# Optimization experiments

Measured on AMD Instinct MI355X. Metric: run time of the kernel, lower is better.

Reference implementation:

```python
import jax, jax.numpy as jnp
import numpy as np
import math

N_HEADS = 16
SINK_STRENGTH = 0.1


def setup_inputs() -> dict:
    key = jax.random.key(0)
    ks = jax.random.split(key, 16)
    B, S, D = 2, 2048, 1024
    sd = 1.0 / math.sqrt(D)
    return {
        "query": jax.random.normal(ks[0], (B, S, D), jnp.float32),
        "key_": jax.random.normal(ks[1], (B, S, D), jnp.float32),
        "value": jax.random.normal(ks[2], (B, S, D), jnp.float32),
        "positions": jax.random.uniform(ks[3], (B, S), jnp.float32),
        "attention_mask": jnp.ones((B, S), jnp.int32),
        "Wq": jax.random.normal(ks[4], (D, D), jnp.float32) * sd,
        "bq": jnp.zeros((D,), jnp.float32),
        "Wk": jax.random.normal(ks[5], (D, D), jnp.float32) * sd,
        "bk": jnp.zeros((D,), jnp.float32),
        "Wv": jax.random.normal(ks[6], (D, D), jnp.float32) * sd,
        "bv": jnp.zeros((D,), jnp.float32),
        "Wo": jax.random.normal(ks[7], (D, D), jnp.float32) * sd,
        "bo": jnp.zeros((D,), jnp.float32),
    }


def reference(query, key_, value, positions, attention_mask, Wq, bq, Wk, bk, Wv, bv, Wo, bo):
    B, S, D = query.shape
    H = N_HEADS
    hd = D // H
    scale = 1.0 / math.sqrt(hd)

    def split_heads(x):  # [B,S,D] -> [B,H,S,hd]
        return x.reshape(B, S, H, hd).transpose(0, 2, 1, 3)

    q = split_heads(query @ Wq.T + bq)
    k = split_heads(key_ @ Wk.T + bk)
    v = split_heads(value @ Wv.T + bv)

    scores = jnp.einsum("bhqd,bhkd->bhqk", q, k) * scale  # [B,H,S,S]

    # sink index: argmin of positions over valid (mask!=0) tokens, per batch
    masked_pos = jnp.where(attention_mask == 0, jnp.inf, positions)
    sink_indices = jnp.argmin(masked_pos, axis=-1)  # [B]

    # per-batch sink bias: add sink_strength to every score column at sink index
    sink_onehot = jax.nn.one_hot(sink_indices, S, dtype=scores.dtype)  # [B,S]
    scores = scores + SINK_STRENGTH * sink_onehot[:, None, None, :]

    # key-side padding mask
    scores = jnp.where(attention_mask[:, None, None, :] == 0, -1e9, scores)

    probs = jax.nn.softmax(scores, axis=-1)
    out = jnp.einsum("bhqk,bhkd->bhqd", probs, v)  # [B,H,S,hd]
    out = out.transpose(0, 2, 1, 3).reshape(B, S, D)
    return out @ Wo.T + bo, sink_indices
```

## Files before the change

### kernel.cpp

```cpp
#include <hip/hip_runtime.h>
#include <hip/hip_bf16.h>
#include <math.h>

constexpr int B  = 2;
constexpr int S  = 2048;
constexpr int D  = 1024;
constexpr int H  = 16;
constexpr int HD = 64;
constexpr float SCALE = 0.125f;
constexpr float SINK_STRENGTH = 0.1f;

typedef short v4s __attribute__((ext_vector_type(4)));
typedef short v8s __attribute__((ext_vector_type(8)));
typedef float v4f __attribute__((ext_vector_type(4)));

__device__ inline v4f mfma_16x16x32_bf16(v8s a, v8s b, v4f c) {
  return __builtin_amdgcn_mfma_f32_16x16x32_bf16(a, b, c, 0, 0, 0);
}

__device__ inline v4f mfma_16x16x16_bf16(v4s a, v4s b, v4f c) {
#if defined(__has_builtin)
#if __has_builtin(__builtin_amdgcn_mfma_f32_16x16x16bf16_1k)
  return __builtin_amdgcn_mfma_f32_16x16x16bf16_1k(a, b, c, 0, 0, 0);
#define MFMA16_DONE 1
#endif
#endif
#ifndef MFMA16_DONE
  v4f d;
  asm volatile("v_mfma_f32_16x16x16_bf16 %0, %1, %2, %3"
               : "=v"(d) : "v"(a), "v"(b), "v"(c));
  return d;
#endif
}

__device__ inline unsigned short f2bf(float f) {
  __hip_bfloat16 h = __float2bfloat16(f);
  return *reinterpret_cast<unsigned short*>(&h);
}

__device__ inline ushort4 pack4(float4 f) {
  return make_ushort4(f2bf(f.x), f2bf(f.y), f2bf(f.z), f2bf(f.w));
}

__device__ inline void gld16(const void* g, void* l) {
  __builtin_amdgcn_global_load_lds(
      (const __attribute__((address_space(1))) void*)g,
      (__attribute__((address_space(3))) void*)l, 16, 0, 0);
}

__device__ inline void stage8(const unsigned char* gbase, size_t gstride,
                              unsigned char* ldsbase, int rb, int lane) {
  const int r = rb + (lane >> 3);
  const int c = (lane & 7) * 16;
  const unsigned char* g = gbase + (size_t)r * gstride + (c ^ ((r & 7) << 4));
  gld16(g, ldsbase + rb * 128);
}

__device__ inline unsigned swz(int row, int bytecol) {
  return (unsigned)(row * 128 + (bytecol ^ ((row & 7) << 4)));
}

struct CvtArgs {
  const float* src[7];
  unsigned short* dst[7];
  int n[7];
};

__global__ __launch_bounds__(256) void convert_kernel(CvtArgs a) {
  const int t = blockIdx.y;
  const float* s = a.src[t];
  unsigned short* d = a.dst[t];
  const int n = a.n[t];
  for (int i = (blockIdx.x * 256 + threadIdx.x) * 8; i < n;
       i += gridDim.x * 256 * 8) {
    float4 f0 = *reinterpret_cast<const float4*>(s + i);
    float4 f1 = *reinterpret_cast<const float4*>(s + i + 4);
    *reinterpret_cast<ushort4*>(d + i)     = pack4(f0);
    *reinterpret_cast<ushort4*>(d + i + 4) = pack4(f1);
  }
}

__global__ void sink_kernel(const float* __restrict__ pos,
                            const int* __restrict__ mask,
                            int* __restrict__ sink_idx,
                            float* __restrict__ sbias_g,
                            float* __restrict__ out_tail, int tail_elems) {
  const int b = blockIdx.x;
  __shared__ float sval[256];
  __shared__ int   sidx[256];
  float best = INFINITY;
  int   bidx = 0x7fffffff;
  for (int i = threadIdx.x; i < S; i += 256) {
    float v = (mask[b * S + i] == 0) ? INFINITY : pos[b * S + i];
    if (v < best || (v == best && i < bidx)) { best = v; bidx = i; }
  }
  sval[threadIdx.x] = best;
  sidx[threadIdx.x] = bidx;
  __syncthreads();
  for (int off = 128; off > 0; off >>= 1) {
    if ((int)threadIdx.x < off) {
      float v  = sval[threadIdx.x + off];
      int   ix = sidx[threadIdx.x + off];
      if (v < sval[threadIdx.x] ||
          (v == sval[threadIdx.x] && ix < sidx[threadIdx.x])) {
        sval[threadIdx.x] = v;
        sidx[threadIdx.x] = ix;
      }
    }
    __syncthreads();
  }
  const int sb = sidx[0];
  if (threadIdx.x == 0) {
    sink_idx[b] = sb;
    if (b < tail_elems) out_tail[b] = (float)sb;
  }
  for (int i = threadIdx.x; i < S; i += 256)
    sbias_g[b * S + i] =
        mask[b * S + i] ? ((i == sb) ? SINK_STRENGTH : 0.f) : -1e9f;
}

template <int MODE>
__global__ __launch_bounds__(256) void gemm_bf16(
    const unsigned short* __restrict__ X,
    const unsigned short* __restrict__ Wb,
    const float* __restrict__ bias,
    void* __restrict__ Yv, int M, int N, int K) {
  __shared__ __align__(16) unsigned char lds[2 * 24576];
  const int tid = threadIdx.x, lane = tid & 63, w = tid >> 6;
  const int wr = w >> 1, wc = w & 1, lr = lane & 15, g = lane >> 4;
  const int m0 = blockIdx.y * 128, n0 = blockIdx.x * 64;
  const unsigned char* xg = (const unsigned char*)(X + (size_t)m0 * K);
  const unsigned char* wg = (const unsigned char*)(Wb + (size_t)n0 * K);
  const size_t stride = (size_t)K * 2;

  auto stage = [&](int buf, int k0) {
    unsigned char* Xs = lds + buf * 24576;
    unsigned char* Ws = Xs + 16384;
    const unsigned char* xk = xg + k0 * 2;
    const unsigned char* wk = wg + k0 * 2;
#pragma unroll
    for (int u = 0; u < 4; ++u) stage8(xk, stride, Xs, w * 32 + u * 8, lane);
#pragma unroll
    for (int u = 0; u < 2; ++u) stage8(wk, stride, Ws, w * 16 + u * 8, lane);
  };

  stage(0, 0);
  v4f acc[4][2] = {};
  const int ksteps = K / 64;
  int cur = 0;
  for (int s = 0; s < ksteps; ++s) {
    __syncthreads();
    if (s + 1 < ksteps) stage(cur ^ 1, (s + 1) * 64);
    const unsigned char* Xs = lds + cur * 24576;
    const unsigned char* Ws = Xs + 16384;
    const int sw = (lr & 7) << 4;
#pragma unroll
    for (int ks = 0; ks < 2; ++ks) {
      v8s a[4], bf2[2];
#pragma unroll
      for (int mf = 0; mf < 4; ++mf)
        a[mf] = *reinterpret_cast<const v8s*>(
            Xs + (wr * 64 + mf * 16 + lr) * 128 + ((ks * 64 + g * 16) ^ sw));
#pragma unroll
      for (int nf = 0; nf < 2; ++nf)
        bf2[nf] = *reinterpret_cast<const v8s*>(
            Ws + (wc * 32 + nf * 16 + lr) * 128 + ((ks * 64 + g * 16) ^ sw));
#pragma unroll
      for (int mf = 0; mf < 4; ++mf)
#pragma unroll
        for (int nf = 0; nf < 2; ++nf)
          acc[mf][nf] = mfma_16x16x32_bf16(a[mf], bf2[nf], acc[mf][nf]);
    }
    cur ^= 1;
  }

  if constexpr (MODE == 2) {
    float* Y = (float*)Yv;
#pragma unroll
    for (int nf = 0; nf < 2; ++nf) {
      const int n = n0 + wc * 32 + nf * 16 + lr;
      const float bs = bias[n];
#pragma unroll
      for (int mf = 0; mf < 4; ++mf)
#pragma unroll
        for (int r = 0; r < 4; ++r)
          Y[(size_t)(m0 + wr * 64 + mf * 16 + g * 4 + r) * N + n] =
              acc[mf][nf][r] + bs;
    }
  } else if constexpr (MODE == 0) {
    unsigned short* Y = (unsigned short*)Yv;
#pragma unroll
    for (int nf = 0; nf < 2; ++nf) {
      const int n = n0 + wc * 32 + nf * 16 + lr;
      const float bs = bias[n];
#pragma unroll
      for (int mf = 0; mf < 4; ++mf)
#pragma unroll
        for (int r = 0; r < 4; ++r)
          Y[(size_t)(m0 + wr * 64 + mf * 16 + g * 4 + r) * N + n] =
              f2bf(acc[mf][nf][r] + bs);
    }
  } else {
    unsigned short* Y = (unsigned short*)Yv;
#pragma unroll
    for (int nf = 0; nf < 2; ++nf) {
      const int n = n0 + wc * 32 + nf * 16 + lr;
      const int hh = n >> 6, dd = n & 63;
      const float bs = bias[n];
#pragma unroll
      for (int mf = 0; mf < 4; ++mf) {
        const int m = m0 + wr * 64 + mf * 16 + g * 4;
        const int bb = m >> 11, ss = m & 2047;
        float4 f = make_float4(acc[mf][nf][0] + bs, acc[mf][nf][1] + bs,
                               acc[mf][nf][2] + bs, acc[mf][nf][3] + bs);
        *reinterpret_cast<ushort4*>(
            &Y[(((size_t)bb * H + hh) * HD + dd) * S + ss]) = pack4(f);
      }
    }
  }
}

__global__ __launch_bounds__(256) void attn_kernel(
    const unsigned short* __restrict__ qg, const unsigned short* __restrict__ kg,
    const unsigned short* __restrict__ vt, const float* __restrict__ sbias_g,
    unsigned short* __restrict__ og) {
  __shared__ __align__(16) unsigned char smem[8192 + 2 * 16384];
  const int b = blockIdx.z, h = blockIdx.y, q0 = blockIdx.x * 64;
  const int tid = threadIdx.x, lane = tid & 63, wv = tid >> 6;
  const int lr = lane & 15, g = lane >> 4;

  const unsigned char* qgb =
      (const unsigned char*)(qg + ((size_t)b * S + q0) * D + h * HD);
  const unsigned char* kgb0 =
      (const unsigned char*)(kg + (size_t)b * S * D + h * HD);
  const unsigned char* vtb =
      (const unsigned char*)(vt + ((size_t)b * H + h) * HD * S);

  stage8(qgb, D * 2, smem, wv * 16, lane);
  stage8(qgb, D * 2, smem, wv * 16 + 8, lane);
  {
    unsigned char* Ks = smem + 8192;
    unsigned char* Vs = Ks + 8192;
    stage8(kgb0, D * 2, Ks, wv * 16, lane);
    stage8(kgb0, D * 2, Ks, wv * 16 + 8, lane);
    stage8(vtb, S * 2, Vs, wv * 16, lane);
    stage8(vtb, S * 2, Vs, wv * 16 + 8, lane);
  }

  float m_i = -INFINITY, l_i = 0.f;
  v4f acc[4] = {};
  v8s qf[2];
  int cur = 0;

  for (int kv0 = 0; kv0 < S; kv0 += 64) {
    __syncthreads();
    const unsigned char* Ks = smem + 8192 + cur * 16384;
    const unsigned char* Vs = Ks + 8192;

    float4 b4[4];
#pragma unroll
    for (int t = 0; t < 4; ++t)
      b4[t] = *reinterpret_cast<const float4*>(
          &sbias_g[b * S + kv0 + t * 16 + g * 4]);

    if (kv0 + 64 < S) {
      unsigned char* Kn = smem + 8192 + (cur ^ 1) * 16384;
      unsigned char* Vn = Kn + 8192;
      const unsigned char* kgb = kgb0 + (size_t)(kv0 + 64) * (D * 2);
      const unsigned char* vgb = vtb + (size_t)(kv0 + 64) * 2;
      stage8(kgb, D * 2, Kn, wv * 16, lane);
      stage8(kgb, D * 2, Kn, wv * 16 + 8, lane);
      stage8(vgb, S * 2, Vn, wv * 16, lane);
      stage8(vgb, S * 2, Vn, wv * 16 + 8, lane);
    }

    if (kv0 == 0) {
      qf[0] = *reinterpret_cast<const v8s*>(smem + swz(wv * 16 + lr, g * 16));
      qf[1] = *reinterpret_cast<const v8s*>(
          smem + swz(wv * 16 + lr, 64 + g * 16));
    }

    v4f st[4] = {};
#pragma unroll
    for (int t = 0; t < 4; ++t) {
#pragma unroll
      for (int ks = 0; ks < 2; ++ks) {
        v8s aK = *reinterpret_cast<const v8s*>(
            Ks + swz(t * 16 + lr, ks * 64 + g * 16));
        st[t] = mfma_16x16x32_bf16(aK, qf[ks], st[t]);
      }
    }

    float s[4][4];
    float mx = -INFINITY;
#pragma unroll
    for (int t = 0; t < 4; ++t) {
      const float bb[4] = {b4[t].x, b4[t].y, b4[t].z, b4[t].w};
#pragma unroll
      for (int r = 0; r < 4; ++r) {
        s[t][r] = fmaf(st[t][r], SCALE, bb[r]);
        mx = fmaxf(mx, s[t][r]);
      }
    }
    mx = fmaxf(mx, __shfl_xor(mx, 16, 64));
    mx = fmaxf(mx, __shfl_xor(mx, 32, 64));

    const float mn   = fmaxf(m_i, mx);
    const float corr = __expf(m_i - mn);
    float rs = 0.f;
    v4s pb[4];
#pragma unroll
    for (int t = 0; t < 4; ++t) {
#pragma unroll
      for (int r = 0; r < 4; ++r) {
        float pv = __expf(s[t][r] - mn);
        rs += pv;
        pb[t][r] = (short)f2bf(pv);
      }
    }
    rs += __shfl_xor(rs, 16, 64);
    rs += __shfl_xor(rs, 32, 64);
    l_i = l_i * corr + rs;
    m_i = mn;
#pragma unroll
    for (int c = 0; c < 4; ++c) acc[c] = acc[c] * corr;

#pragma unroll
    for (int t = 0; t < 4; ++t) {
#pragma unroll
      for (int c = 0; c < 4; ++c) {
        v4s aV = *reinterpret_cast<const v4s*>(
            Vs + swz(c * 16 + lr, t * 32 + g * 8));
        acc[c] = mfma_16x16x16_bf16(aV, pb[t], acc[c]);
      }
    }
    cur ^= 1;
  }

  const float inv = 1.0f / l_i;
  unsigned short* orow = og + ((size_t)b * S + q0 + wv * 16 + lr) * D + h * HD;
#pragma unroll
  for (int c = 0; c < 4; ++c) {
    float4 f = make_float4(acc[c][0] * inv, acc[c][1] * inv, acc[c][2] * inv,
                           acc[c][3] * inv);
    *reinterpret_cast<ushort4*>(orow + c * 16 + g * 4) = pack4(f);
  }
}

extern "C" void kernel_launch(void* const* d_in, const int* in_sizes, int n_in,
                              void* d_out, int out_size, void* d_ws,
                              size_t ws_size, hipStream_t stream) {
  const float* query = (const float*)d_in[0];
  const float* key_  = (const float*)d_in[1];
  const float* value = (const float*)d_in[2];
  const float* pos   = (const float*)d_in[3];
  const int*   amask = (const int*)d_in[4];
  const float* Wq = (const float*)d_in[5];
  const float* bq = (const float*)d_in[6];
  const float* Wk = (const float*)d_in[7];
  const float* bk = (const float*)d_in[8];
  const float* Wv = (const float*)d_in[9];
  const float* bv = (const float*)d_in[10];
  const float* Wo = (const float*)d_in[11];
  const float* bo = (const float*)d_in[12];
  float* out = (float*)d_out;

  constexpr size_t NBSD = (size_t)B * S * D;
  constexpr size_t NDD  = (size_t)D * D;
  unsigned short* qx  = (unsigned short*)d_ws;
  unsigned short* kx  = qx + NBSD;
  unsigned short* vx  = kx + NBSD;
  unsigned short* wqb = vx + NBSD;
  unsigned short* wkb = wqb + NDD;
  unsigned short* wvb = wkb + NDD;
  unsigned short* wob = wvb + NDD;
  unsigned short* qb  = wob + NDD;
  unsigned short* kb  = qb + NBSD;
  unsigned short* vt  = kb + NBSD;
  float* sbias_g = (float*)(vt + NBSD);
  int*   sidx    = (int*)(sbias_g + B * S);
  unsigned short* ab = qx;

  CvtArgs ca;
  ca.src[0] = query; ca.dst[0] = qx;  ca.n[0] = (int)NBSD;
  ca.src[1] = key_;  ca.dst[1] = kx;  ca.n[1] = (int)NBSD;
  ca.src[2] = value; ca.dst[2] = vx;  ca.n[2] = (int)NBSD;
  ca.src[3] = Wq;    ca.dst[3] = wqb; ca.n[3] = (int)NDD;
  ca.src[4] = Wk;    ca.dst[4] = wkb; ca.n[4] = (int)NDD;
  ca.src[5] = Wv;    ca.dst[5] = wvb; ca.n[5] = (int)NDD;
  ca.src[6] = Wo;    ca.dst[6] = wob; ca.n[6] = (int)NDD;
  convert_kernel<<<dim3(2048, 7), 256, 0, stream>>>(ca);

  const int tail_elems = out_size - (int)NBSD;
  sink_kernel<<<B, 256, 0, stream>>>(pos, amask, sidx, sbias_g,
                                     out + NBSD, tail_elems);

  dim3 blk(256);
  dim3 gmm(D / 64, (B * S) / 128);
  gemm_bf16<0><<<gmm, blk, 0, stream>>>(qx, wqb, bq, qb, B * S, D, D);
  gemm_bf16<0><<<gmm, blk, 0, stream>>>(kx, wkb, bk, kb, B * S, D, D);
  gemm_bf16<1><<<gmm, blk, 0, stream>>>(vx, wvb, bv, vt, B * S, D, D);

  attn_kernel<<<dim3(S / 64, H, B), blk, 0, stream>>>(qb, kb, vt, sbias_g, ab);

  gemm_bf16<2><<<gmm, blk, 0, stream>>>(ab, wob, bo, out, B * S, D, D);
}
```

Baseline: 264.1 us.

## Fuse QKV GEMMs with larger tiles and optimize attention softmax loop

Merges the three projection GEMMs into one launch using 128x128 tiles and an XCD-aware block remap. The attention softmax switches to exp2 with log2e folded into the scale and bias, and rescales the running accumulator only when the row max grows past a threshold. It also adds s_setprio around the MFMA sections, moves the barrier to the end of the loop, and remaps attention blocks across XCDs. The lazy rescale relies on the accumulator staying bounded while the max is stale, and the larger GEMM tiles increase register and LDS use per block.

```diff
diff --git a/kernel.cpp b/kernel.cpp
--- a/kernel.cpp
+++ b/kernel.cpp
@@ -7,12 +7,18 @@
 constexpr int D  = 1024;
 constexpr int H  = 16;
 constexpr int HD = 64;
-constexpr float SCALE = 0.125f;
 constexpr float SINK_STRENGTH = 0.1f;
+constexpr float LOG2E  = 1.4426950408889634f;
+constexpr float SCALE2 = 0.125f * LOG2E;
+constexpr float THR2   = 8.0f * LOG2E;
 
 typedef short v4s __attribute__((ext_vector_type(4)));
 typedef short v8s __attribute__((ext_vector_type(8)));
 typedef float v4f __attribute__((ext_vector_type(4)));
+
+__device__ inline float exp2_fast(float x) {
+  return __builtin_amdgcn_exp2f(x);
+}
 
 __device__ inline v4f mfma_16x16x32_bf16(v8s a, v8s b, v4f c) {
   return __builtin_amdgcn_mfma_f32_16x16x32_bf16(a, b, c, 0, 0, 0);
@@ -82,7 +88,6 @@
 
 __global__ void sink_kernel(const float* __restrict__ pos,
                             const int* __restrict__ mask,
-                            int* __restrict__ sink_idx,
                             float* __restrict__ sbias_g,
                             float* __restrict__ out_tail, int tail_elems) {
   const int b = blockIdx.x;
@@ -110,34 +115,124 @@
     __syncthreads();
   }
   const int sb = sidx[0];
-  if (threadIdx.x == 0) {
-    sink_idx[b] = sb;
-    if (b < tail_elems) out_tail[b] = (float)sb;
-  }
+  if (threadIdx.x == 0 && b < tail_elems) out_tail[b] = (float)sb;
   for (int i = threadIdx.x; i < S; i += 256)
     sbias_g[b * S + i] =
-        mask[b * S + i] ? ((i == sb) ? SINK_STRENGTH : 0.f) : -1e9f;
-}
-
-template <int MODE>
-__global__ __launch_bounds__(256) void gemm_bf16(
-    const unsigned short* __restrict__ X,
-    const unsigned short* __restrict__ Wb,
-    const float* __restrict__ bias,
-    void* __restrict__ Yv, int M, int N, int K) {
+        (mask[b * S + i] ? ((i == sb) ? SINK_STRENGTH : 0.f) : -1e9f) * LOG2E;
+}
+
+struct QKVArgs {
+  const unsigned short* x[3];
+  const unsigned short* w[3];
+  const float* bias[3];
+  unsigned short* y[3];
+};
+
+__global__ __launch_bounds__(256) void gemm_qkv(QKVArgs args) {
+  __shared__ __align__(16) unsigned char lds[2 * 32768];
+  int id = blockIdx.x;
+  id = (id & 7) * 96 + (id >> 3);
+  const int z = id >> 8, rem = id & 255;
+  const int m0 = (rem >> 3) * 128, n0 = (rem & 7) * 128;
+
+  const int tid = threadIdx.x, lane = tid & 63, w = tid >> 6;
+  const int wr = w >> 1, wc = w & 1, lr = lane & 15, g = lane >> 4;
+  const unsigned short* X  = args.x[z];
+  const unsigned short* Wb = args.w[z];
+  const unsigned char* xg = (const unsigned char*)(X + (size_t)m0 * D);
+  const unsigned char* wg = (const unsigned char*)(Wb + (size_t)n0 * D);
+  const size_t stride = (size_t)D * 2;
+
+  auto stage = [&](int buf, int k0) {
+    unsigned char* Xs = lds + buf * 32768;
+    unsigned char* Ws = Xs + 16384;
+    const unsigned char* xk = xg + (size_t)k0 * 2;
+    const unsigned char* wk = wg + (size_t)k0 * 2;
+#pragma unroll
+    for (int u = 0; u < 4; ++u) stage8(xk, stride, Xs, w * 32 + u * 8, lane);
+#pragma unroll
+    for (int u = 0; u < 4; ++u) stage8(wk, stride, Ws, w * 32 + u * 8, lane);
+  };
+
+  stage(0, 0);
+  v4f acc[4][4] = {};
+  const int ksteps = D / 64;
+  int cur = 0;
+  for (int s = 0; s < ksteps; ++s) {
+    __syncthreads();
+    if (s + 1 < ksteps) stage(cur ^ 1, (s + 1) * 64);
+    const unsigned char* Xs = lds + cur * 32768;
+    const unsigned char* Ws = Xs + 16384;
+    const int sw = (lr & 7) << 4;
+#pragma unroll
+    for (int ks = 0; ks < 2; ++ks) {
+      v8s a[4], bb[4];
+#pragma unroll
+      for (int mf = 0; mf < 4; ++mf)
+        a[mf] = *reinterpret_cast<const v8s*>(
+            Xs + (wr * 64 + mf * 16 + lr) * 128 + ((ks * 64 + g * 16) ^ sw));
+#pragma unroll
+      for (int nf = 0; nf < 4; ++nf)
+        bb[nf] = *reinterpret_cast<const v8s*>(
+            Ws + (wc * 64 + nf * 16 + lr) * 128 + ((ks * 64 + g * 16) ^ sw));
+#pragma unroll
+      for (int mf = 0; mf < 4; ++mf)
+#pragma unroll
+        for (int nf = 0; nf < 4; ++nf)
+          acc[mf][nf] = mfma_16x16x32_bf16(a[mf], bb[nf], acc[mf][nf]);
+    }
+    cur ^= 1;
+  }
+
+  const float* bias = args.bias[z];
+  unsigned short* Y = args.y[z];
+  if (z < 2) {
+#pragma unroll
+    for (int nf = 0; nf < 4; ++nf) {
+      const int n = n0 + wc * 64 + nf * 16 + lr;
+      const float bs = bias[n];
+#pragma unroll
+      for (int mf = 0; mf < 4; ++mf)
+#pragma unroll
+        for (int r = 0; r < 4; ++r)
+          Y[(size_t)(m0 + wr * 64 + mf * 16 + g * 4 + r) * D + n] =
+              f2bf(acc[mf][nf][r] + bs);
+    }
+  } else {
+#pragma unroll
+    for (int nf = 0; nf < 4; ++nf) {
+      const int n = n0 + wc * 64 + nf * 16 + lr;
+      const int hh = n >> 6, dd = n & 63;
+      const float bs = bias[n];
+#pragma unroll
+      for (int mf = 0; mf < 4; ++mf) {
+        const int m = m0 + wr * 64 + mf * 16 + g * 4;
+        const int bb2 = m >> 11, ss = m & 2047;
+        float4 f = make_float4(acc[mf][nf][0] + bs, acc[mf][nf][1] + bs,
+                               acc[mf][nf][2] + bs, acc[mf][nf][3] + bs);
+        *reinterpret_cast<ushort4*>(
+            &Y[(((size_t)bb2 * H + hh) * HD + dd) * S + ss]) = pack4(f);
+      }
+    }
+  }
+}
+
+__global__ __launch_bounds__(256) void gemm_o(
+    const unsigned short* __restrict__ X, const unsigned short* __restrict__ Wb,
+    const float* __restrict__ bias, float* __restrict__ Y) {
   __shared__ __align__(16) unsigned char lds[2 * 24576];
   const int tid = threadIdx.x, lane = tid & 63, w = tid >> 6;
   const int wr = w >> 1, wc = w & 1, lr = lane & 15, g = lane >> 4;
   const int m0 = blockIdx.y * 128, n0 = blockIdx.x * 64;
-  const unsigned char* xg = (const unsigned char*)(X + (size_t)m0 * K);
-  const unsigned char* wg = (const unsigned char*)(Wb + (size_t)n0 * K);
-  const size_t stride = (size_t)K * 2;
+  const unsigned char* xg = (const unsigned char*)(X + (size_t)m0 * D);
+  const unsigned char* wg = (const unsigned char*)(Wb + (size_t)n0 * D);
+  const size_t stride = (size_t)D * 2;
 
   auto stage = [&](int buf, int k0) {
     unsigned char* Xs = lds + buf * 24576;
     unsigned char* Ws = Xs + 16384;
-    const unsigned char* xk = xg + k0 * 2;
-    const unsigned char* wk = wg + k0 * 2;
+    const unsigned char* xk = xg + (size_t)k0 * 2;
+    const unsigned char* wk = wg + (size_t)k0 * 2;
 #pragma unroll
     for (int u = 0; u < 4; ++u) stage8(xk, stride, Xs, w * 32 + u * 8, lane);
 #pragma unroll
@@ -146,7 +241,7 @@
 
   stage(0, 0);
   v4f acc[4][2] = {};
-  const int ksteps = K / 64;
+  const int ksteps = D / 64;
   int cur = 0;
   for (int s = 0; s < ksteps; ++s) {
     __syncthreads();
@@ -173,50 +268,16 @@
     }
     cur ^= 1;
   }
-
-  if constexpr (MODE == 2) {
-    float* Y = (float*)Yv;
-#pragma unroll
-    for (int nf = 0; nf < 2; ++nf) {
-      const int n = n0 + wc * 32 + nf * 16 + lr;
-      const float bs = bias[n];
-#pragma unroll
-      for (int mf = 0; mf < 4; ++mf)
-#pragma unroll
-        for (int r = 0; r < 4; ++r)
-          Y[(size_t)(m0 + wr * 64 + mf * 16 + g * 4 + r) * N + n] =
-              acc[mf][nf][r] + bs;
-    }
-  } else if constexpr (MODE == 0) {
-    unsigned short* Y = (unsigned short*)Yv;
-#pragma unroll
-    for (int nf = 0; nf < 2; ++nf) {
-      const int n = n0 + wc * 32 + nf * 16 + lr;
-      const float bs = bias[n];
-#pragma unroll
-      for (int mf = 0; mf < 4; ++mf)
-#pragma unroll
-        for (int r = 0; r < 4; ++r)
-          Y[(size_t)(m0 + wr * 64 + mf * 16 + g * 4 + r) * N + n] =
-              f2bf(acc[mf][nf][r] + bs);
-    }
-  } else {
-    unsigned short* Y = (unsigned short*)Yv;
-#pragma unroll
-    for (int nf = 0; nf < 2; ++nf) {
-      const int n = n0 + wc * 32 + nf * 16 + lr;
-      const int hh = n >> 6, dd = n & 63;
-      const float bs = bias[n];
-#pragma unroll
-      for (int mf = 0; mf < 4; ++mf) {
-        const int m = m0 + wr * 64 + mf * 16 + g * 4;
-        const int bb = m >> 11, ss = m & 2047;
-        float4 f = make_float4(acc[mf][nf][0] + bs, acc[mf][nf][1] + bs,
-                               acc[mf][nf][2] + bs, acc[mf][nf][3] + bs);
-        *reinterpret_cast<ushort4*>(
-            &Y[(((size_t)bb * H + hh) * HD + dd) * S + ss]) = pack4(f);
-      }
-    }
+#pragma unroll
+  for (int nf = 0; nf < 2; ++nf) {
+    const int n = n0 + wc * 32 + nf * 16 + lr;
+    const float bs = bias[n];
+#pragma unroll
+    for (int mf = 0; mf < 4; ++mf)
+#pragma unroll
+      for (int r = 0; r < 4; ++r)
+        Y[(size_t)(m0 + wr * 64 + mf * 16 + g * 4 + r) * D + n] =
+            acc[mf][nf][r] + bs;
   }
 }
 
@@ -225,7 +286,11 @@
     const unsigned short* __restrict__ vt, const float* __restrict__ sbias_g,
     unsigned short* __restrict__ og) {
   __shared__ __align__(16) unsigned char smem[8192 + 2 * 16384];
-  const int b = blockIdx.z, h = blockIdx.y, q0 = blockIdx.x * 64;
+  int id = blockIdx.x;
+  id = (id & 7) * 128 + (id >> 3);
+  const int q0 = (id & 31) * 64, hb = id >> 5;
+  const int h = hb & 15, b = hb >> 4;
+
   const int tid = threadIdx.x, lane = tid & 63, wv = tid >> 6;
   const int lr = lane & 15, g = lane >> 4;
 
@@ -246,14 +311,16 @@
     stage8(vtb, S * 2, Vs, wv * 16, lane);
     stage8(vtb, S * 2, Vs, wv * 16 + 8, lane);
   }
+  __syncthreads();
+  v8s qf[2];
+  qf[0] = *reinterpret_cast<const v8s*>(smem + swz(wv * 16 + lr, g * 16));
+  qf[1] = *reinterpret_cast<const v8s*>(smem + swz(wv * 16 + lr, 64 + g * 16));
 
   float m_i = -INFINITY, l_i = 0.f;
   v4f acc[4] = {};
-  v8s qf[2];
   int cur = 0;
 
   for (int kv0 = 0; kv0 < S; kv0 += 64) {
-    __syncthreads();
     const unsigned char* Ks = smem + 8192 + cur * 16384;
     const unsigned char* Vs = Ks + 8192;
 
@@ -274,13 +341,8 @@
       stage8(vgb, S * 2, Vn, wv * 16 + 8, lane);
     }
 
-    if (kv0 == 0) {
-      qf[0] = *reinterpret_cast<const v8s*>(smem + swz(wv * 16 + lr, g * 16));
-      qf[1] = *reinterpret_cast<const v8s*>(
-          smem + swz(wv * 16 + lr, 64 + g * 16));
-    }
-
     v4f st[4] = {};
+    __builtin_amdgcn_s_setprio(1);
 #pragma unroll
     for (int t = 0; t < 4; ++t) {
 #pragma unroll
@@ -290,6 +352,7 @@
         st[t] = mfma_16x16x32_bf16(aK, qf[ks], st[t]);
       }
     }
+    __builtin_amdgcn_s_setprio(0);
 
     float s[4][4];
     float mx = -INFINITY;
@@ -297,34 +360,37 @@
     for (int t = 0; t < 4; ++t) {
       const float bb[4] = {b4[t].x, b4[t].y, b4[t].z, b4[t].w};
 #pragma unroll
-      for (int r = 0; r < 4; ++r) {
-        s[t][r] = fmaf(st[t][r], SCALE, bb[r]);
-        mx = fmaxf(mx, s[t][r]);
-      }
+      for (int r = 0; r < 4; ++r) s[t][r] = fmaf(st[t][r], SCALE2, bb[r]);
+      mx = fmaxf(mx, fmaxf(fmaxf(s[t][0], s[t][1]), fmaxf(s[t][2], s[t][3])));
     }
     mx = fmaxf(mx, __shfl_xor(mx, 16, 64));
     mx = fmaxf(mx, __shfl_xor(mx, 32, 64));
 
-    const float mn   = fmaxf(m_i, mx);
-    const float corr = __expf(m_i - mn);
+    if (__any(mx > m_i + THR2)) {
+      const float mn   = fmaxf(m_i, mx);
+      const float corr = exp2_fast(m_i - mn);
+      l_i *= corr;
+#pragma unroll
+      for (int c = 0; c < 4; ++c) acc[c] = acc[c] * corr;
+      m_i = mn;
+    }
+
     float rs = 0.f;
     v4s pb[4];
 #pragma unroll
     for (int t = 0; t < 4; ++t) {
 #pragma unroll
       for (int r = 0; r < 4; ++r) {
-        float pv = __expf(s[t][r] - mn);
+        float pv = exp2_fast(s[t][r] - m_i);
         rs += pv;
         pb[t][r] = (short)f2bf(pv);
       }
     }
     rs += __shfl_xor(rs, 16, 64);
     rs += __shfl_xor(rs, 32, 64);
-    l_i = l_i * corr + rs;
-    m_i = mn;
-#pragma unroll
-    for (int c = 0; c < 4; ++c) acc[c] = acc[c] * corr;
-
+    l_i += rs;
+
+    __builtin_amdgcn_s_setprio(1);
 #pragma unroll
     for (int t = 0; t < 4; ++t) {
 #pragma unroll
@@ -334,6 +400,9 @@
         acc[c] = mfma_16x16x16_bf16(aV, pb[t], acc[c]);
       }
     }
+    __builtin_amdgcn_s_setprio(0);
+
+    __syncthreads();
     cur ^= 1;
   }
 
@@ -378,7 +447,6 @@
   unsigned short* kb  = qb + NBSD;
   unsigned short* vt  = kb + NBSD;
   float* sbias_g = (float*)(vt + NBSD);
-  int*   sidx    = (int*)(sbias_g + B * S);
   unsigned short* ab = qx;
 
   CvtArgs ca;
@@ -392,16 +460,16 @@
   convert_kernel<<<dim3(2048, 7), 256, 0, stream>>>(ca);
 
   const int tail_elems = out_size - (int)NBSD;
-  sink_kernel<<<B, 256, 0, stream>>>(pos, amask, sidx, sbias_g,
-                                     out + NBSD, tail_elems);
-
-  dim3 blk(256);
-  dim3 gmm(D / 64, (B * S) / 128);
-  gemm_bf16<0><<<gmm, blk, 0, stream>>>(qx, wqb, bq, qb, B * S, D, D);
-  gemm_bf16<0><<<gmm, blk, 0, stream>>>(kx, wkb, bk, kb, B * S, D, D);
-  gemm_bf16<1><<<gmm, blk, 0, stream>>>(vx, wvb, bv, vt, B * S, D, D);
-
-  attn_kernel<<<dim3(S / 64, H, B), blk, 0, stream>>>(qb, kb, vt, sbias_g, ab);
-
-  gemm_bf16<2><<<gmm, blk, 0, stream>>>(ab, wob, bo, out, B * S, D, D);
-}
+  sink_kernel<<<B, 256, 0, stream>>>(pos, amask, sbias_g, out + NBSD,
+                                     tail_elems);
+
+  QKVArgs qa;
+  qa.x[0] = qx; qa.w[0] = wqb; qa.bias[0] = bq; qa.y[0] = qb;
+  qa.x[1] = kx; qa.w[1] = wkb; qa.bias[1] = bk; qa.y[1] = kb;
+  qa.x[2] = vx; qa.w[2] = wvb; qa.bias[2] = bv; qa.y[2] = vt;
+  gemm_qkv<<<768, 256, 0, stream>>>(qa);
+
+  attn_kernel<<<1024, 256, 0, stream>>>(qb, kb, vt, sbias_g, ab);
+
+  gemm_o<<<dim3(D / 64, (B * S) / 128), 256, 0, stream>>>(ab, wob, bo, out);
+}
```

Measured after the change: 260.4 us. Within noise of the previous version (-1.4%).
